# Performance work log

Hardware: AMD Instinct MI355X
Metric: run time of the kernel (lower is better)

## Reference

```python
import jax, jax.numpy as jnp
import numpy as np

RADIUS = 0.1
K_NEIGHBOURS = 32


def setup_inputs() -> dict:
    key = jax.random.key(0)
    k1, k2, k3 = jax.random.split(key, 3)
    B, N, M, C = 4, 8192, 2048, 128
    xyz = jax.random.uniform(k1, (B, 3, N), dtype=jnp.float32)
    new_xyz = jax.random.uniform(k2, (B, 3, M), dtype=jnp.float32)
    feature = jax.random.normal(k3, (B, C, N), dtype=jnp.float32)
    return {"new_xyz": new_xyz, "xyz": xyz, "feature": feature, "use_xyz": 1}


def _ball_query(xyz, new_xyz, radius, k):
    # xyz: [B,3,N], new_xyz: [B,3,M] -> idx [B,M,k] (first-k-in-ball, padded
    # with first valid index, pointnet2 semantics), counts [B,M]
    n = xyz.shape[-1]
    # squared pairwise distance [B,M,N]
    d2 = jnp.sum((new_xyz[:, :, :, None] - xyz[:, :, None, :]) ** 2, axis=1)
    in_ball = d2 < radius * radius
    cand = jnp.where(in_ball, jnp.arange(n, dtype=jnp.int32), n)
    # smallest indices first == first-k points inside the ball
    idx_sorted = jnp.sort(cand, axis=-1)[..., :k]
    valid = idx_sorted < n
    first = idx_sorted[..., :1]
    pad = jnp.where(first < n, first, 0)  # empty ball -> index 0
    idx = jnp.where(valid, idx_sorted, pad).astype(jnp.int32)
    count = jnp.sum(valid, axis=-1).astype(jnp.int32)
    return idx, count


def _group_points(f, idx):
    # f: [B,C,N], idx: [B,M,K] -> [B,C,M,K]
    return jax.vmap(lambda fb, ib: fb[:, ib])(f, idx)


def reference(new_xyz, xyz, feature, use_xyz):
    idx, _count = _ball_query(xyz, new_xyz, RADIUS, K_NEIGHBOURS)
    group_xyz = _group_points(xyz, idx) - new_xyz[..., None]  # [B,3,M,K]
    group_feature = _group_points(feature, idx)               # [B,C,M,K]
    if use_xyz:
        group_feature = jnp.concatenate([group_xyz, group_feature], axis=1)
    return group_feature, group_xyz
```

## Files before the change

### kernel.cpp

```cpp
#include <hip/hip_runtime.h>
#include <hip/hip_bf16.h>


#define K_NEIGH 32
#define R2_F32 0.009999999776482582f
#define CCH 128
#define NPTS 8192
#define MQ 2048

__global__ __launch_bounds__(512) void ball_lds_kernel(
    const float* __restrict__ xyz,
    const float* __restrict__ new_xyz,
    int* __restrict__ idxb,
    float* __restrict__ out0,
    float* __restrict__ out1,
    int use_xyz)
{
    constexpr int CH = 2048;
    __shared__ float sx[CH], sy[CH], sz[CH];
    __shared__ int lidx[8][K_NEIGH];

    const int tid  = threadIdx.x;
    const int wave = tid >> 6;
    const int lane = tid & 63;
    const int q = blockIdx.x * 8 + wave;
    const int b = q / MQ;
    const int m = q - b * MQ;

    const float* x0 = xyz + (size_t)b * 3 * NPTS;
    const float* x1 = x0 + NPTS;
    const float* x2 = x1 + NPTS;
    const float* nb = new_xyz + (size_t)b * 3 * MQ;
    const float qx = nb[m];
    const float qy = nb[MQ + m];
    const float qz = nb[2 * MQ + m];

    int cnt = 0;
    int ff  = 0;
    const unsigned long long below = (1ull << lane) - 1ull;

    for (int c0 = 0; c0 < NPTS; c0 += CH) {
        const int i4 = tid * 4;
        *(float4*)&sx[i4] = *(const float4*)&x0[c0 + i4];
        *(float4*)&sy[i4] = *(const float4*)&x1[c0 + i4];
        *(float4*)&sz[i4] = *(const float4*)&x2[c0 + i4];
        __syncthreads();

        for (int g = 0; g < CH; g += 256) {
            const int i = g + lane;
            const float ax0 = sx[i];       const float ay0 = sy[i];       const float az0 = sz[i];
            const float ax1 = sx[i + 64];  const float ay1 = sy[i + 64];  const float az1 = sz[i + 64];
            const float ax2 = sx[i + 128]; const float ay2 = sy[i + 128]; const float az2 = sz[i + 128];
            const float ax3 = sx[i + 192]; const float ay3 = sy[i + 192]; const float az3 = sz[i + 192];

            #define D2(ax, ay, az) \
                __fadd_rn(__fadd_rn(__fmul_rn((ax) - qx, (ax) - qx), \
                                    __fmul_rn((ay) - qy, (ay) - qy)), \
                          __fmul_rn((az) - qz, (az) - qz))
            const bool in0 = D2(ax0, ay0, az0) < R2_F32;
            const bool in1 = D2(ax1, ay1, az1) < R2_F32;
            const bool in2 = D2(ax2, ay2, az2) < R2_F32;
            const bool in3 = D2(ax3, ay3, az3) < R2_F32;
            #undef D2

            const unsigned long long m0 = __ballot(in0);
            const unsigned long long m1 = __ballot(in1);
            const unsigned long long m2 = __ballot(in2);
            const unsigned long long m3 = __ballot(in3);

            const int gi = c0 + g + lane;
            #define SUBIT(mm, inn, ii)                                        \
                if (mm) {                                                     \
                    if (cnt == 0) ff = (ii) - lane + (__ffsll(mm) - 1);       \
                    if (inn) {                                                \
                        const int pos = cnt + __popcll((mm) & below);         \
                        if (pos < K_NEIGH) lidx[wave][pos] = (ii);            \
                    }                                                         \
                    cnt += __popcll(mm);                                      \
                }
            SUBIT(m0, in0, gi)
            SUBIT(m1, in1, gi + 64)
            SUBIT(m2, in2, gi + 128)
            SUBIT(m3, in3, gi + 192)
            #undef SUBIT
        }
        __syncthreads();
    }

    asm volatile("s_waitcnt lgkmcnt(0)" ::: "memory");

    if (lane < K_NEIGH) {
        const int j = (lane < cnt) ? lidx[wave][lane] : ff;
        idxb[(size_t)q * K_NEIGH + lane] = j;
        const float gx = x0[j] - qx;
        const float gy = x1[j] - qy;
        const float gz = x2[j] - qz;
        const size_t MK = (size_t)MQ * K_NEIGH;
        const size_t o1 = (size_t)b * 3 * MK + (size_t)m * K_NEIGH + lane;
        out1[o1]          = gx;
        out1[o1 + MK]     = gy;
        out1[o1 + 2 * MK] = gz;
        if (use_xyz) {
            const size_t o0 = (size_t)b * (CCH + 3) * MK + (size_t)m * K_NEIGH + lane;
            out0[o0]          = gx;
            out0[o0 + MK]     = gy;
            out0[o0 + 2 * MK] = gz;
        }
    }
}

__global__ __launch_bounds__(256) void ball_query_xyz_kernel(
    const float* __restrict__ xyz, const float* __restrict__ new_xyz,
    int* __restrict__ idxb, float* __restrict__ out0, float* __restrict__ out1,
    int N, int M, int C, int use_xyz)
{
    __shared__ int lidx[4][K_NEIGH];
    const int wave = threadIdx.x >> 6;
    const int lane = threadIdx.x & 63;
    const int q = blockIdx.x * 4 + wave;
    const int b = q / M;
    const int m = q - b * M;

    const float* xb = xyz + (size_t)b * 3 * N;
    const float* x0 = xb;
    const float* x1 = xb + N;
    const float* x2 = xb + 2 * N;
    const float* nb = new_xyz + (size_t)b * 3 * M;
    const float qx = nb[m];
    const float qy = nb[M + m];
    const float qz = nb[2 * M + m];

    int cnt = 0;
    int ff  = 0;
    const unsigned long long below = (1ull << lane) - 1ull;

    for (int t0 = 0; t0 < N; t0 += 64) {
        const int i = t0 + lane;
        const float dx = x0[i] - qx;
        const float dy = x1[i] - qy;
        const float dz = x2[i] - qz;
        const float d2 = __fadd_rn(__fadd_rn(__fmul_rn(dx, dx), __fmul_rn(dy, dy)),
                                   __fmul_rn(dz, dz));
        const bool in_ball = d2 < R2_F32;
        const unsigned long long mask = __ballot(in_ball);
        if (mask) {
            if (cnt == 0) ff = t0 + (__ffsll(mask) - 1);
            if (in_ball) {
                const int pos = cnt + __popcll(mask & below);
                if (pos < K_NEIGH) lidx[wave][pos] = i;
            }
            cnt += __popcll(mask);
            if (cnt >= K_NEIGH) break;
        }
    }

    asm volatile("s_waitcnt lgkmcnt(0)" ::: "memory");

    if (lane < K_NEIGH) {
        const int j = (lane < cnt) ? lidx[wave][lane] : ff;
        idxb[(size_t)q * K_NEIGH + lane] = j;
        const float gx = x0[j] - qx;
        const float gy = x1[j] - qy;
        const float gz = x2[j] - qz;
        const size_t MK = (size_t)M * K_NEIGH;
        const size_t o1 = (size_t)b * 3 * MK + (size_t)m * K_NEIGH + lane;
        out1[o1]          = gx;
        out1[o1 + MK]     = gy;
        out1[o1 + 2 * MK] = gz;
        if (use_xyz) {
            const size_t o0 = (size_t)b * (C + 3) * MK + (size_t)m * K_NEIGH + lane;
            out0[o0]          = gx;
            out0[o0 + MK]     = gy;
            out0[o0 + 2 * MK] = gz;
        }
    }
}

__global__ __launch_bounds__(1024, 4) void gather_onepass_kernel(
    const float* __restrict__ feat,
    const int* __restrict__ idxb,
    float* __restrict__ out0,
    int use_xyz)
{
    __shared__ float sf[2 * NPTS];

    const int t   = threadIdx.x;
    const int bid = blockIdx.x;
    const int b   = (bid & 7) >> 1;
    const int cg  = ((bid >> 3) << 1) | (bid & 1);
    const int c0  = cg * 2;

    const int4* ip4 = (const int4*)(idxb + (size_t)b * MQ * K_NEIGH);
    int4 jj[16];
    #pragma unroll
    for (int i = 0; i < 16; ++i) jj[i] = ip4[i * 1024 + t];

    const float4* fv = (const float4*)(feat + ((size_t)b * CCH + c0) * NPTS);
    #pragma unroll
    for (int r = 0; r < 4; ++r)
        ((float4*)sf)[t + r * 1024] = fv[t + r * 1024];
    __syncthreads();

    const size_t MK = (size_t)MQ * K_NEIGH;
    const int CO   = use_xyz ? (CCH + 3) : CCH;
    const int coff = use_xyz ? 3 : 0;
    float* o0 = out0 + ((size_t)b * CO + coff + c0) * MK;
    float* o1 = o0 + MK;

    #pragma unroll
    for (int i = 0; i < 16; ++i) {
        const int p = i * 4096 + 4 * t;
        const int4 j4 = jj[i];
        float4 s0, s1;
        s0.x = sf[j4.x]; s0.y = sf[j4.y]; s0.z = sf[j4.z]; s0.w = sf[j4.w];
        s1.x = sf[NPTS + j4.x]; s1.y = sf[NPTS + j4.y];
        s1.z = sf[NPTS + j4.z]; s1.w = sf[NPTS + j4.w];
        *(float4*)(o0 + p) = s0;
        *(float4*)(o1 + p) = s1;
    }
}

__global__ __launch_bounds__(256) void gather_kernel(
    const float* __restrict__ xyz, const float* __restrict__ new_xyz,
    const float* __restrict__ feat, const int* __restrict__ idxb,
    float* __restrict__ out0, float* __restrict__ out1,
    int N, int M, int C, int use_xyz)
{
    const int tid = threadIdx.x;
    const int k = tid & 31;
    const int mloc = tid >> 5;
    const int mchunks = M >> 3;
    const int b = blockIdx.x / mchunks;
    const int m = (blockIdx.x - b * mchunks) * 8 + mloc;
    const int q = b * M + m;
    const int j = idxb[(size_t)q * K_NEIGH + k];
    const size_t xb = (size_t)b * 3 * N;
    const size_t nb = (size_t)b * 3 * M;
    const float gx = xyz[xb + j]         - new_xyz[nb + m];
    const float gy = xyz[xb + N + j]     - new_xyz[nb + M + m];
    const float gz = xyz[xb + 2 * N + j] - new_xyz[nb + 2 * M + m];
    const size_t MK = (size_t)M * K_NEIGH;
    const size_t o1 = (size_t)b * 3 * MK + (size_t)m * K_NEIGH + k;
    out1[o1] = gx; out1[o1 + MK] = gy; out1[o1 + 2 * MK] = gz;
    const int CO = use_xyz ? (C + 3) : C;
    size_t o0 = (size_t)b * CO * MK + (size_t)m * K_NEIGH + k;
    if (use_xyz) {
        out0[o0] = gx; out0[o0 + MK] = gy; out0[o0 + 2 * MK] = gz;
        o0 += 3 * MK;
    }
    const float* fb = feat + (size_t)b * C * N;
    #pragma unroll 4
    for (int c = 0; c < C; c += 4) {
        const float v0 = fb[(size_t)c * N + j];
        const float v1 = fb[(size_t)(c + 1) * N + j];
        const float v2 = fb[(size_t)(c + 2) * N + j];
        const float v3 = fb[(size_t)(c + 3) * N + j];
        out0[o0 + (size_t)c * MK]       = v0;
        out0[o0 + (size_t)(c + 1) * MK] = v1;
        out0[o0 + (size_t)(c + 2) * MK] = v2;
        out0[o0 + (size_t)(c + 3) * MK] = v3;
    }
}

extern "C" void kernel_launch(void* const* d_in, const int* in_sizes, int n_in,
                              void* d_out, int out_size, void* d_ws, size_t ws_size,
                              hipStream_t stream) {
    const float* new_xyz = (const float*)d_in[0];
    const float* xyz     = (const float*)d_in[1];
    const float* feat    = (const float*)d_in[2];

    const int B = 4;
    const int M = in_sizes[0] / (3 * B);
    const int N = in_sizes[1] / (3 * B);
    const int C = in_sizes[2] / (B * N);

    const long long sz_with = (long long)B * (C + 6) * M * K_NEIGH;
    const int use_xyz = (out_size == sz_with) ? 1 : 0;

    float* out0 = (float*)d_out;
    float* out1 = out0 + (size_t)B * (use_xyz ? (C + 3) : C) * M * K_NEIGH;

    int* idxb = (int*)d_ws;
    const size_t idx_bytes = (size_t)B * M * K_NEIGH * sizeof(int);

    const bool fast = (B == 4) && (N == NPTS) && (M == MQ) && (C == CCH)
                      && (ws_size >= idx_bytes);

    if (fast) {
        ball_lds_kernel<<<(B * M) / 8, 512, 0, stream>>>(
            xyz, new_xyz, idxb, out0, out1, use_xyz);
        gather_onepass_kernel<<<256, 1024, 0, stream>>>(feat, idxb, out0, use_xyz);
    } else {
        ball_query_xyz_kernel<<<(B * M) / 4, 256, 0, stream>>>(
            xyz, new_xyz, idxb, out0, out1, N, M, C, use_xyz);
        gather_kernel<<<B * (M / 8), 256, 0, stream>>>(xyz, new_xyz, feat, idxb,
                                                       out0, out1, N, M, C, use_xyz);
    }
}
```

Measured before the change: 53.21 us.

## Process four queries per wave with packed float4 LDS points and early exit

Each wave now handles four query points instead of one, so every LDS point load is reused across four distance tests, and the grid shrinks by four. Points are packed into a float4 AoS layout in shared memory so one wide LDS read fetches x, y and z together. A chunk's scan is skipped once all four queries already hold 32 neighbours. In exchange the kernel uses more registers per thread and launches fewer blocks, which may reduce occupancy and parallelism for the ball-query phase.

```diff
diff --git a/kernel.cpp b/kernel.cpp
--- a/kernel.cpp
+++ b/kernel.cpp
@@ -8,7 +8,7 @@
 #define NPTS 8192
 #define MQ 2048
 
-__global__ __launch_bounds__(512) void ball_lds_kernel(
+__global__ __launch_bounds__(512, 8) void ball_q4_kernel(
     const float* __restrict__ xyz,
     const float* __restrict__ new_xyz,
     int* __restrict__ idxb,
@@ -17,94 +17,108 @@
     int use_xyz)
 {
     constexpr int CH = 2048;
-    __shared__ float sx[CH], sy[CH], sz[CH];
-    __shared__ int lidx[8][K_NEIGH];
+    __shared__ float4 pts[CH];
+    __shared__ int lidx[8][4][K_NEIGH];
 
     const int tid  = threadIdx.x;
     const int wave = tid >> 6;
     const int lane = tid & 63;
-    const int q = blockIdx.x * 8 + wave;
-    const int b = q / MQ;
-    const int m = q - b * MQ;
+    const int q0 = blockIdx.x * 32 + wave * 4;
+    const int b  = q0 / MQ;
+    const int m0 = q0 - b * MQ;
 
     const float* x0 = xyz + (size_t)b * 3 * NPTS;
     const float* x1 = x0 + NPTS;
     const float* x2 = x1 + NPTS;
     const float* nb = new_xyz + (size_t)b * 3 * MQ;
-    const float qx = nb[m];
-    const float qy = nb[MQ + m];
-    const float qz = nb[2 * MQ + m];
-
-    int cnt = 0;
-    int ff  = 0;
+
+    float qx[4], qy[4], qz[4];
+    int   cnt[4] = {0, 0, 0, 0};
+    int   ff [4] = {0, 0, 0, 0};
+    #pragma unroll
+    for (int j = 0; j < 4; ++j) {
+        qx[j] = nb[m0 + j];
+        qy[j] = nb[MQ + m0 + j];
+        qz[j] = nb[2 * MQ + m0 + j];
+    }
     const unsigned long long below = (1ull << lane) - 1ull;
 
     for (int c0 = 0; c0 < NPTS; c0 += CH) {
-        const int i4 = tid * 4;
-        *(float4*)&sx[i4] = *(const float4*)&x0[c0 + i4];
-        *(float4*)&sy[i4] = *(const float4*)&x1[c0 + i4];
-        *(float4*)&sz[i4] = *(const float4*)&x2[c0 + i4];
+        {
+            const int p0 = tid * 4;
+            const float4 vx = *(const float4*)&x0[c0 + p0];
+            const float4 vy = *(const float4*)&x1[c0 + p0];
+            const float4 vz = *(const float4*)&x2[c0 + p0];
+            pts[p0 + 0] = make_float4(vx.x, vy.x, vz.x, 0.f);
+            pts[p0 + 1] = make_float4(vx.y, vy.y, vz.y, 0.f);
+            pts[p0 + 2] = make_float4(vx.z, vy.z, vz.z, 0.f);
+            pts[p0 + 3] = make_float4(vx.w, vy.w, vz.w, 0.f);
+        }
         __syncthreads();
 
-        for (int g = 0; g < CH; g += 256) {
-            const int i = g + lane;
-            const float ax0 = sx[i];       const float ay0 = sy[i];       const float az0 = sz[i];
-            const float ax1 = sx[i + 64];  const float ay1 = sy[i + 64];  const float az1 = sz[i + 64];
-            const float ax2 = sx[i + 128]; const float ay2 = sy[i + 128]; const float az2 = sz[i + 128];
-            const float ax3 = sx[i + 192]; const float ay3 = sy[i + 192]; const float az3 = sz[i + 192];
-
-            #define D2(ax, ay, az) \
-                __fadd_rn(__fadd_rn(__fmul_rn((ax) - qx, (ax) - qx), \
-                                    __fmul_rn((ay) - qy, (ay) - qy)), \
-                          __fmul_rn((az) - qz, (az) - qz))
-            const bool in0 = D2(ax0, ay0, az0) < R2_F32;
-            const bool in1 = D2(ax1, ay1, az1) < R2_F32;
-            const bool in2 = D2(ax2, ay2, az2) < R2_F32;
-            const bool in3 = D2(ax3, ay3, az3) < R2_F32;
-            #undef D2
-
-            const unsigned long long m0 = __ballot(in0);
-            const unsigned long long m1 = __ballot(in1);
-            const unsigned long long m2 = __ballot(in2);
-            const unsigned long long m3 = __ballot(in3);
-
-            const int gi = c0 + g + lane;
-            #define SUBIT(mm, inn, ii)                                        \
-                if (mm) {                                                     \
-                    if (cnt == 0) ff = (ii) - lane + (__ffsll(mm) - 1);       \
-                    if (inn) {                                                \
-                        const int pos = cnt + __popcll((mm) & below);         \
-                        if (pos < K_NEIGH) lidx[wave][pos] = (ii);            \
-                    }                                                         \
-                    cnt += __popcll(mm);                                      \
+        const bool alldone = (cnt[0] >= K_NEIGH) && (cnt[1] >= K_NEIGH) &&
+                             (cnt[2] >= K_NEIGH) && (cnt[3] >= K_NEIGH);
+        if (!alldone) {
+            for (int g = 0; g < CH; g += 128) {
+                const float4 pa = pts[g + lane];
+                const float4 pb = pts[g + 64 + lane];
+                const int gia = c0 + g + lane;
+
+                #pragma unroll
+                for (int j = 0; j < 4; ++j) {
+                    #define D2(P) \
+                        __fadd_rn(__fadd_rn(__fmul_rn((P).x - qx[j], (P).x - qx[j]), \
+                                            __fmul_rn((P).y - qy[j], (P).y - qy[j])), \
+                                  __fmul_rn((P).z - qz[j], (P).z - qz[j]))
+                    const bool ina = D2(pa) < R2_F32;
+                    const bool inb = D2(pb) < R2_F32;
+                    #undef D2
+                    const unsigned long long ma = __ballot(ina);
+                    const unsigned long long mb = __ballot(inb);
+                    if (ma) {
+                        if (cnt[j] == 0) ff[j] = gia - lane + (__ffsll(ma) - 1);
+                        if (ina) {
+                            const int pos = cnt[j] + __popcll(ma & below);
+                            if (pos < K_NEIGH) lidx[wave][j][pos] = gia;
+                        }
+                        cnt[j] += __popcll(ma);
+                    }
+                    if (mb) {
+                        if (cnt[j] == 0) ff[j] = gia - lane + 64 + (__ffsll(mb) - 1);
+                        if (inb) {
+                            const int pos = cnt[j] + __popcll(mb & below);
+                            if (pos < K_NEIGH) lidx[wave][j][pos] = gia + 64;
+                        }
+                        cnt[j] += __popcll(mb);
+                    }
                 }
-            SUBIT(m0, in0, gi)
-            SUBIT(m1, in1, gi + 64)
-            SUBIT(m2, in2, gi + 128)
-            SUBIT(m3, in3, gi + 192)
-            #undef SUBIT
+            }
         }
         __syncthreads();
     }
 
     asm volatile("s_waitcnt lgkmcnt(0)" ::: "memory");
 
-    if (lane < K_NEIGH) {
-        const int j = (lane < cnt) ? lidx[wave][lane] : ff;
-        idxb[(size_t)q * K_NEIGH + lane] = j;
-        const float gx = x0[j] - qx;
-        const float gy = x1[j] - qy;
-        const float gz = x2[j] - qz;
-        const size_t MK = (size_t)MQ * K_NEIGH;
-        const size_t o1 = (size_t)b * 3 * MK + (size_t)m * K_NEIGH + lane;
-        out1[o1]          = gx;
-        out1[o1 + MK]     = gy;
-        out1[o1 + 2 * MK] = gz;
-        if (use_xyz) {
-            const size_t o0 = (size_t)b * (CCH + 3) * MK + (size_t)m * K_NEIGH + lane;
-            out0[o0]          = gx;
-            out0[o0 + MK]     = gy;
-            out0[o0 + 2 * MK] = gz;
+    const size_t MK = (size_t)MQ * K_NEIGH;
+    #pragma unroll
+    for (int j = 0; j < 4; ++j) {
+        if (lane < K_NEIGH) {
+            const int m = m0 + j;
+            const int jdx = (lane < cnt[j]) ? lidx[wave][j][lane] : ff[j];
+            idxb[((size_t)b * MQ + m) * K_NEIGH + lane] = jdx;
+            const float gx = x0[jdx] - qx[j];
+            const float gy = x1[jdx] - qy[j];
+            const float gz = x2[jdx] - qz[j];
+            const size_t o1 = (size_t)b * 3 * MK + (size_t)m * K_NEIGH + lane;
+            out1[o1]          = gx;
+            out1[o1 + MK]     = gy;
+            out1[o1 + 2 * MK] = gz;
+            if (use_xyz) {
+                const size_t o0 = (size_t)b * (CCH + 3) * MK + (size_t)m * K_NEIGH + lane;
+                out0[o0]          = gx;
+                out0[o0 + MK]     = gy;
+                out0[o0 + 2 * MK] = gz;
+            }
         }
     }
 }
@@ -287,7 +301,7 @@
                       && (ws_size >= idx_bytes);
 
     if (fast) {
-        ball_lds_kernel<<<(B * M) / 8, 512, 0, stream>>>(
+        ball_q4_kernel<<<(B * MQ) / 32, 512, 0, stream>>>(
             xyz, new_xyz, idxb, out0, out1, use_xyz);
         gather_onepass_kernel<<<256, 1024, 0, stream>>>(feat, idxb, out0, use_xyz);
     } else {
```

New measurement: 64.23 us. +20.7%, slower.

## Bin points by x-slab and scan only nearby bins in ball query

Applied to the files above, without the earlier changes.

Adds a pre-pass kernel that bucket-sorts each batch's points into 16 slabs along x, storing packed float4 coordinates plus the original index. The ball query then scans only the slabs overlapping the query's x range instead of all 8192 points. Hits are gathered and bitonic-sorted by original index so the first-k ordering is preserved. If more than 64 hits are found, it falls back to a full linear scan with early exit. This cuts distance work by roughly the slab fraction, at the cost of an extra launch and a single-block-per-batch binning kernel whose serial latency may dominate.

```diff
diff --git a/kernel.cpp b/kernel.cpp
--- a/kernel.cpp
+++ b/kernel.cpp
@@ -7,25 +7,64 @@
 #define CCH 128
 #define NPTS 8192
 #define MQ 2048
-
-__global__ __launch_bounds__(512) void ball_lds_kernel(
+#define NBIN 16
+
+__global__ __launch_bounds__(1024) void bin_points_kernel(
     const float* __restrict__ xyz,
-    const float* __restrict__ new_xyz,
-    int* __restrict__ idxb,
-    float* __restrict__ out0,
-    float* __restrict__ out1,
+    float4* __restrict__ binned,
+    int* __restrict__ binStart)
+{
+    __shared__ int hist[NBIN];
+    __shared__ int start[NBIN + 1];
+    __shared__ int cursor[NBIN];
+    const int t = threadIdx.x;
+    const int b = blockIdx.x;
+    const float* x0 = xyz + (size_t)b * 3 * NPTS;
+    const float* x1 = x0 + NPTS;
+    const float* x2 = x1 + NPTS;
+
+    if (t < NBIN) hist[t] = 0;
+    __syncthreads();
+    #pragma unroll
+    for (int k = 0; k < NPTS / 1024; ++k) {
+        const int i = t + k * 1024;
+        int bin = (int)floorf(x0[i] * 16.0f);
+        bin = bin < 0 ? 0 : (bin > 15 ? 15 : bin);
+        atomicAdd(&hist[bin], 1);
+    }
+    __syncthreads();
+    if (t == 0) {
+        int acc = 0;
+        for (int k = 0; k < NBIN; ++k) { start[k] = acc; cursor[k] = acc; acc += hist[k]; }
+        start[NBIN] = acc;
+    }
+    __syncthreads();
+    #pragma unroll
+    for (int k = 0; k < NPTS / 1024; ++k) {
+        const int i = t + k * 1024;
+        const float x = x0[i];
+        int bin = (int)floorf(x * 16.0f);
+        bin = bin < 0 ? 0 : (bin > 15 ? 15 : bin);
+        const int slot = atomicAdd(&cursor[bin], 1);
+        float4 p;
+        p.x = x; p.y = x1[i]; p.z = x2[i]; p.w = __int_as_float(i);
+        binned[(size_t)b * NPTS + slot] = p;
+    }
+    if (t <= NBIN) binStart[b * (NBIN + 1) + t] = start[t];
+}
+
+__global__ __launch_bounds__(256, 8) void ball_binned_kernel(
+    const float* __restrict__ xyz, const float* __restrict__ new_xyz,
+    const float4* __restrict__ binned, const int* __restrict__ binStart,
+    int* __restrict__ idxb, float* __restrict__ out0, float* __restrict__ out1,
     int use_xyz)
 {
-    constexpr int CH = 2048;
-    __shared__ float sx[CH], sy[CH], sz[CH];
-    __shared__ int lidx[8][K_NEIGH];
-
-    const int tid  = threadIdx.x;
-    const int wave = tid >> 6;
-    const int lane = tid & 63;
-    const int q = blockIdx.x * 8 + wave;
-    const int b = q / MQ;
-    const int m = q - b * MQ;
+    __shared__ int sidx[4][64];
+    const int wav  = threadIdx.x >> 6;
+    const int lane = threadIdx.x & 63;
+    const int q = blockIdx.x * 4 + wav;
+    const int b = q >> 11;
+    const int m = q & (MQ - 1);
 
     const float* x0 = xyz + (size_t)b * 3 * NPTS;
     const float* x1 = x0 + NPTS;
@@ -35,62 +74,82 @@
     const float qy = nb[MQ + m];
     const float qz = nb[2 * MQ + m];
 
-    int cnt = 0;
-    int ff  = 0;
+    int lo = (int)floorf((qx - 0.100001f) * 16.0f);
+    int hi = (int)floorf((qx + 0.100001f) * 16.0f);
+    lo = lo < 0 ? 0 : (lo > 15 ? 15 : lo);
+    hi = hi < 0 ? 0 : (hi > 15 ? 15 : hi);
+    const int s = binStart[b * (NBIN + 1) + lo];
+    const int e = binStart[b * (NBIN + 1) + hi + 1];
+    const float4* bp = binned + (size_t)b * NPTS;
+
     const unsigned long long below = (1ull << lane) - 1ull;
-
-    for (int c0 = 0; c0 < NPTS; c0 += CH) {
-        const int i4 = tid * 4;
-        *(float4*)&sx[i4] = *(const float4*)&x0[c0 + i4];
-        *(float4*)&sy[i4] = *(const float4*)&x1[c0 + i4];
-        *(float4*)&sz[i4] = *(const float4*)&x2[c0 + i4];
-        __syncthreads();
-
-        for (int g = 0; g < CH; g += 256) {
-            const int i = g + lane;
-            const float ax0 = sx[i];       const float ay0 = sy[i];       const float az0 = sz[i];
-            const float ax1 = sx[i + 64];  const float ay1 = sy[i + 64];  const float az1 = sz[i + 64];
-            const float ax2 = sx[i + 128]; const float ay2 = sy[i + 128]; const float az2 = sz[i + 128];
-            const float ax3 = sx[i + 192]; const float ay3 = sy[i + 192]; const float az3 = sz[i + 192];
-
-            #define D2(ax, ay, az) \
-                __fadd_rn(__fadd_rn(__fmul_rn((ax) - qx, (ax) - qx), \
-                                    __fmul_rn((ay) - qy, (ay) - qy)), \
-                          __fmul_rn((az) - qz, (az) - qz))
-            const bool in0 = D2(ax0, ay0, az0) < R2_F32;
-            const bool in1 = D2(ax1, ay1, az1) < R2_F32;
-            const bool in2 = D2(ax2, ay2, az2) < R2_F32;
-            const bool in3 = D2(ax3, ay3, az3) < R2_F32;
-            #undef D2
-
-            const unsigned long long m0 = __ballot(in0);
-            const unsigned long long m1 = __ballot(in1);
-            const unsigned long long m2 = __ballot(in2);
-            const unsigned long long m3 = __ballot(in3);
-
-            const int gi = c0 + g + lane;
-            #define SUBIT(mm, inn, ii)                                        \
-                if (mm) {                                                     \
-                    if (cnt == 0) ff = (ii) - lane + (__ffsll(mm) - 1);       \
-                    if (inn) {                                                \
-                        const int pos = cnt + __popcll((mm) & below);         \
-                        if (pos < K_NEIGH) lidx[wave][pos] = (ii);            \
-                    }                                                         \
-                    cnt += __popcll(mm);                                      \
+    int hcnt = 0;
+    for (int g = s; g < e; g += 64) {
+        const int i = g + lane;
+        bool hit = false;
+        int oi = 0;
+        if (i < e) {
+            const float4 p = bp[i];
+            const float d2 = __fadd_rn(__fadd_rn(__fmul_rn(p.x - qx, p.x - qx),
+                                                 __fmul_rn(p.y - qy, p.y - qy)),
+                                       __fmul_rn(p.z - qz, p.z - qz));
+            hit = d2 < R2_F32;
+            oi = __float_as_int(p.w);
+        }
+        const unsigned long long mk = __ballot(hit);
+        if (hit) {
+            const int pos = hcnt + (int)__popcll(mk & below);
+            if (pos < 64) sidx[wav][pos] = oi;
+        }
+        hcnt += (int)__popcll(mk);
+    }
+
+    asm volatile("s_waitcnt lgkmcnt(0)" ::: "memory");
+
+    int j = 0;
+    if (hcnt <= 64) {
+        int v = (lane < hcnt) ? sidx[wav][lane] : 0x7FFFFFFF;
+        #pragma unroll
+        for (int k = 2; k <= 64; k <<= 1) {
+            #pragma unroll
+            for (int jj = k >> 1; jj > 0; jj >>= 1) {
+                const int other = __shfl_xor(v, jj, 64);
+                const bool up   = ((lane & k) == 0);
+                const bool lowr = ((lane & jj) == 0);
+                const int mn = v < other ? v : other;
+                const int mx = v < other ? other : v;
+                v = (lowr == up) ? mn : mx;
+            }
+        }
+        const int v0  = __shfl(v, 0, 64);
+        const int pad = (hcnt > 0) ? v0 : 0;
+        j = (lane < hcnt) ? v : pad;
+    } else {
+        int cnt = 0, ff = 0;
+        for (int t0 = 0; t0 < NPTS; t0 += 64) {
+            const int i = t0 + lane;
+            const float dx = x0[i] - qx;
+            const float dy = x1[i] - qy;
+            const float dz = x2[i] - qz;
+            const float d2 = __fadd_rn(__fadd_rn(__fmul_rn(dx, dx), __fmul_rn(dy, dy)),
+                                       __fmul_rn(dz, dz));
+            const bool in_ball = d2 < R2_F32;
+            const unsigned long long mask = __ballot(in_ball);
+            if (mask) {
+                if (cnt == 0) ff = t0 + (__ffsll(mask) - 1);
+                if (in_ball) {
+                    const int pos = cnt + __popcll(mask & below);
+                    if (pos < K_NEIGH) sidx[wav][pos] = i;
                 }
-            SUBIT(m0, in0, gi)
-            SUBIT(m1, in1, gi + 64)
-            SUBIT(m2, in2, gi + 128)
-            SUBIT(m3, in3, gi + 192)
-            #undef SUBIT
-        }
-        __syncthreads();
-    }
-
-    asm volatile("s_waitcnt lgkmcnt(0)" ::: "memory");
+                cnt += __popcll(mask);
+                if (cnt >= K_NEIGH) break;
+            }
+        }
+        asm volatile("s_waitcnt lgkmcnt(0)" ::: "memory");
+        j = (lane < cnt) ? sidx[wav][lane] : ff;
+    }
 
     if (lane < K_NEIGH) {
-        const int j = (lane < cnt) ? lidx[wave][lane] : ff;
         idxb[(size_t)q * K_NEIGH + lane] = j;
         const float gx = x0[j] - qx;
         const float gy = x1[j] - qy;
@@ -281,14 +340,19 @@
     float* out1 = out0 + (size_t)B * (use_xyz ? (C + 3) : C) * M * K_NEIGH;
 
     int* idxb = (int*)d_ws;
-    const size_t idx_bytes = (size_t)B * M * K_NEIGH * sizeof(int);
+    const size_t idx_bytes  = (size_t)B * M * K_NEIGH * sizeof(int);
+    float4* binned = (float4*)((char*)d_ws + idx_bytes);
+    const size_t bin_bytes  = (size_t)B * N * sizeof(float4);
+    int* binStart = (int*)((char*)d_ws + idx_bytes + bin_bytes);
+    const size_t bs_bytes   = (size_t)B * (NBIN + 1) * sizeof(int);
 
     const bool fast = (B == 4) && (N == NPTS) && (M == MQ) && (C == CCH)
-                      && (ws_size >= idx_bytes);
+                      && (ws_size >= idx_bytes + bin_bytes + bs_bytes);
 
     if (fast) {
-        ball_lds_kernel<<<(B * M) / 8, 512, 0, stream>>>(
-            xyz, new_xyz, idxb, out0, out1, use_xyz);
+        bin_points_kernel<<<B, 1024, 0, stream>>>(xyz, binned, binStart);
+        ball_binned_kernel<<<(B * MQ) / 4, 256, 0, stream>>>(
+            xyz, new_xyz, binned, binStart, idxb, out0, out1, use_xyz);
         gather_onepass_kernel<<<256, 1024, 0, stream>>>(feat, idxb, out0, use_xyz);
     } else {
         ball_query_xyz_kernel<<<(B * M) / 4, 256, 0, stream>>>(
```

Result: slower. 56.27 us (+5.7%).
